# Kernel optimization log

Measured on AMD Instinct MI355X. Metric: run time of the kernel, lower is better.

## Reference

```python
import jax, jax.numpy as jnp
import numpy as np

N, E, D_FEAT, D_HID, N_CLASS, N_LAYER = 100000, 1600000, 128, 128, 40, 2


def _sage_layer(x, x_, src, dst, wl, wr, b, n):
    # mean aggregation of neighbor (src) features into dst nodes
    agg = jax.ops.segment_sum(x[src], dst, num_segments=n)          # [N, d_in]
    cnt = jax.ops.segment_sum(jnp.ones((src.shape[0], 1), x.dtype), dst, num_segments=n)
    agg = agg / jnp.maximum(cnt, 1.0)
    h = agg @ wl + x @ wr + b        # neighbor path + root path
    h_ = x_ @ wr + b                 # twin (detached-root) stream: root weight only
    return jax.nn.relu(h), jax.nn.relu(h_)


def setup_inputs() -> dict:
    key = jax.random.key(0)
    ks = jax.random.split(key, 12)
    s = 1.0 / np.sqrt(D_HID)
    inp = {
        "x": jax.random.normal(ks[0], (N, D_FEAT), jnp.float32),
        "edge_index1": jax.random.randint(ks[1], (2, E), 0, N, jnp.int32),
        "edge_index2": jax.random.randint(ks[2], (2, E), 0, N, jnp.int32),
        "wl1": jax.random.uniform(ks[3], (D_FEAT, D_HID), jnp.float32, -s, s),
        "wr1": jax.random.uniform(ks[4], (D_FEAT, D_HID), jnp.float32, -s, s),
        "b1": jnp.zeros((D_HID,), jnp.float32),
        "wl2": jax.random.uniform(ks[5], (D_HID, D_HID), jnp.float32, -s, s),
        "wr2": jax.random.uniform(ks[6], (D_HID, D_HID), jnp.float32, -s, s),
        "b2": jnp.zeros((D_HID,), jnp.float32),
        "w_out": jax.random.uniform(ks[7], (D_HID * N_LAYER, N_CLASS), jnp.float32, -s, s),
        "b_out": jnp.zeros((N_CLASS,), jnp.float32),
        "batch_size": N,
    }
    return inp


def reference(x, edge_index1, edge_index2, wl1, wr1, b1, wl2, wr2, b2, w_out, b_out, batch_size):
    n = x.shape[0]
    x_ = jax.lax.stop_gradient(x)[:batch_size]   # detached twin stream of root nodes
    # layer 1 (dropout is eval-mode no-op)
    h1, h1_ = _sage_layer(x, x_, edge_index1[0], edge_index1[1], wl1, wr1, b1, n)
    # layer 2
    h2, h2_ = _sage_layer(h1, h1_, edge_index2[0], edge_index2[1], wl2, wr2, b2, n)
    # jumping knowledge: mode 'cat' over per-layer root representations
    h = jnp.concatenate([h1[:batch_size], h2[:batch_size]], axis=-1)
    return h @ w_out + b_out
```

## Files before the change

kernel.cpp:

```cpp
#include <hip/hip_runtime.h>


#define MAXB  512
#define CAP   24
#define CAPS  6144
#define PBLK  384

typedef __attribute__((ext_vector_type(8))) short short8;
typedef __attribute__((ext_vector_type(4))) float floatx4;

__device__ __forceinline__ unsigned short f2b(float f) {
    unsigned u = __float_as_uint(f);
    unsigned r = (u + 0x7fffu + ((u >> 16) & 1u)) >> 16;
    return (unsigned short)r;
}
__device__ __forceinline__ float lo2f(unsigned u) { return __uint_as_float(u << 16); }
__device__ __forceinline__ float hi2f(unsigned u) { return __uint_as_float(u & 0xffff0000u); }
__device__ __forceinline__ unsigned pack2(float a, float b) {
    return (unsigned)f2b(a) | ((unsigned)f2b(b) << 16);
}

__global__ __launch_bounds__(256)
void prep_hist(const float4* __restrict__ x4, uint4* __restrict__ xb4, long n8,
               const float* __restrict__ wl1, const float* __restrict__ wr1,
               const float* __restrict__ wl2, const float* __restrict__ wr2,
               const float* __restrict__ wo,
               unsigned short* __restrict__ wt1, unsigned short* __restrict__ wt2,
               unsigned short* __restrict__ wot,
               const int* __restrict__ dst1, const int* __restrict__ dst2,
               int* __restrict__ hist1, int* __restrict__ hist2, int E, int nb) {
    long i = (long)blockIdx.x * 256 + threadIdx.x;
    if (i < n8) {
        float4 a = x4[i * 2];
        float4 b = x4[i * 2 + 1];
        uint4 o;
        o.x = pack2(a.x, a.y); o.y = pack2(a.z, a.w);
        o.z = pack2(b.x, b.y); o.w = pack2(b.z, b.w);
        xb4[i] = o;
    }
    if (i < 65536) {
        int l = (int)(i >> 15);
        int k5 = (int)(i & 32767);
        int j = k5 & 7, lane = (k5 >> 3) & 63, kb = (k5 >> 9) & 7, c = k5 >> 12;
        int k = kb * 32 + (lane >> 4) * 8 + j;
        int n = c * 16 + (lane & 15);
        const float* Wl = l ? wl2 : wl1;
        const float* Wr = l ? wr2 : wr1;
        float v = (k < 128) ? Wl[k * 128 + n] : Wr[(k - 128) * 128 + n];
        (l ? wt2 : wt1)[k5] = f2b(v);
    } else if (i < 65536 + 12288) {
        int k5 = (int)(i - 65536);
        int j = k5 & 7, lane = (k5 >> 3) & 63, kb = (k5 >> 9) & 7, c = k5 >> 12;
        int k = kb * 32 + (lane >> 4) * 8 + j;
        int col = c * 16 + (lane & 15);
        float v = (col < 40) ? wo[k * 40 + col] : 0.0f;
        wot[k5] = f2b(v);
    }
    __shared__ int h[MAXB];
    if (blockIdx.x < 512) {
        const int layer = blockIdx.x >> 8;
        const int bx    = blockIdx.x & 255;
        const int* dst  = layer ? dst2 : dst1;
        int* hist       = layer ? hist2 : hist1;
        for (int k = threadIdx.x; k < nb; k += 256) h[k] = 0;
        __syncthreads();
        for (int e = bx * 256 + threadIdx.x; e < E; e += 256 * 256)
            atomicAdd(&h[dst[e] >> 8], 1);
        __syncthreads();
        for (int k = threadIdx.x; k < nb; k += 256)
            if (h[k]) atomicAdd(&hist[k], h[k]);
    }
}

__global__ __launch_bounds__(256)
void bucket_scan2(const int* __restrict__ hist1, const int* __restrict__ hist2,
                  int* __restrict__ bptr1, int* __restrict__ bptr2, int nb, int E) {
    __shared__ int pair[256];
    const int* hist = blockIdx.x ? hist2 : hist1;
    int* bptr       = blockIdx.x ? bptr2 : bptr1;
    int t = threadIdx.x;
    int v0 = (2 * t < nb) ? hist[2 * t] : 0;
    int v1 = (2 * t + 1 < nb) ? hist[2 * t + 1] : 0;
    pair[t] = v0 + v1;
    __syncthreads();
    for (int off = 1; off < 256; off <<= 1) {
        int y = (t >= off) ? pair[t - off] : 0;
        __syncthreads();
        pair[t] += y;
        __syncthreads();
    }
    int ebase = pair[t] - (v0 + v1);
    if (2 * t < nb)     bptr[2 * t]     = ebase;
    if (2 * t + 1 < nb) bptr[2 * t + 1] = ebase + v0;
    if (t == 0) bptr[nb] = E;
}

__global__ __launch_bounds__(256)
void partition_edges2(const int* __restrict__ ei1, const int* __restrict__ ei2,
                      const int* __restrict__ bptr1, const int* __restrict__ bptr2,
                      int* __restrict__ gcur1, int* __restrict__ gcur2,
                      int* __restrict__ part1, int* __restrict__ part2,
                      int E, int nb) {
    __shared__ unsigned stage[MAXB][CAP];
    __shared__ int lcnt[MAXB];
    const int* src  = blockIdx.y ? ei2 : ei1;
    const int* dst  = src + E;
    const int* bptr = blockIdx.y ? bptr2 : bptr1;
    int* gcur       = blockIdx.y ? gcur2 : gcur1;
    int* part       = blockIdx.y ? part2 : part1;
    const int t = threadIdx.x;
    for (int i = t; i < nb; i += 256) lcnt[i] = 0;
    __syncthreads();
    const int per = (E + gridDim.x - 1) / gridDim.x;
    const int e0 = blockIdx.x * per;
    const int e1 = min(e0 + per, E);
    for (int e = e0 + t; e < e1; e += 256) {
        int d = dst[e];
        int b = d >> 8;
        unsigned rec = (unsigned)src[e] | ((unsigned)(d & 255) << 17);
        int p = atomicAdd(&lcnt[b], 1);
        if (p < CAP) stage[b][p] = rec;
        else {
            int g = atomicAdd(&gcur[b], 1);
            part[bptr[b] + g] = (int)rec;
        }
    }
    __syncthreads();
    for (int b = t; b < nb; b += 256) {
        int c = lcnt[b]; if (c > CAP) c = CAP;
        if (c > 0) {
            int g = atomicAdd(&gcur[b], c);
            int base = bptr[b] + g;
            for (int i = 0; i < c; ++i) part[base + i] = (int)stage[b][i];
        }
    }
}

__global__ __launch_bounds__(256)
void node_sort2(const int* __restrict__ bptr1, const int* __restrict__ bptr2,
                const int* __restrict__ part1, const int* __restrict__ part2,
                int* __restrict__ col1, int* __restrict__ col2,
                int* __restrict__ row_ptr1, int* __restrict__ row_ptr2,
                int N, int E) {
    __shared__ int recs[CAPS];
    __shared__ int sorted[CAPS];
    __shared__ int hcnt[256];
    __shared__ int hoff[256];
    const int* bptr = blockIdx.y ? bptr2 : bptr1;
    const int* part = blockIdx.y ? part2 : part1;
    int* col        = blockIdx.y ? col2 : col1;
    int* row_ptr    = blockIdx.y ? row_ptr2 : row_ptr1;
    const int b = blockIdx.x, t = threadIdx.x;
    const int beg = bptr[b], end = bptr[b + 1];
    int cnt = end - beg;
    if (cnt > CAPS) cnt = CAPS;

    for (int i = t; i < cnt; i += 256) recs[i] = part[beg + i];
    hcnt[t] = 0;
    __syncthreads();
    for (int i = t; i < cnt; i += 256)
        atomicAdd(&hcnt[((unsigned)recs[i]) >> 17], 1);
    __syncthreads();

    int v = hcnt[t];
    hoff[t] = v;
    __syncthreads();
    for (int off = 1; off < 256; off <<= 1) {
        int y = (t >= off) ? hoff[t - off] : 0;
        __syncthreads();
        hoff[t] += y;
        __syncthreads();
    }
    int myoff = hoff[t] - v;

    int row = b * 256 + t;
    if (row <= N) row_ptr[row] = beg + myoff;
    if (b == gridDim.x - 1 && t == 0) row_ptr[N] = E;
    __syncthreads();
    hoff[t] = myoff;
    hcnt[t] = 0;
    __syncthreads();

    for (int i = t; i < cnt; i += 256) {
        unsigned rec = (unsigned)recs[i];
        int node = rec >> 17;
        int p = hoff[node] + atomicAdd(&hcnt[node], 1);
        sorted[p] = (int)(rec & 0x1FFFF);
    }
    __syncthreads();
    for (int i = t; i < cnt; i += 256) col[beg + i] = sorted[i];
}

__device__ __forceinline__ void gather_node(const uint4* __restrict__ xb,
                                            const int* __restrict__ col,
                                            int beg, int end, int lane,
                                            float acc[8]) {
    int e = beg;
    if (e + 8 <= end) {
        int cidx[8];
#pragma unroll
        for (int q = 0; q < 8; ++q) cidx[q] = col[e + q];
        for (;;) {
            uint4 v[8];
#pragma unroll
            for (int q = 0; q < 8; ++q) v[q] = xb[(size_t)cidx[q] * 16 + lane];
            e += 8;
            const bool more = (e + 8 <= end);
            if (more) {
#pragma unroll
                for (int q = 0; q < 8; ++q) cidx[q] = col[e + q];
            }
#pragma unroll
            for (int q = 0; q < 8; ++q) {
                acc[0] += lo2f(v[q].x); acc[1] += hi2f(v[q].x);
                acc[2] += lo2f(v[q].y); acc[3] += hi2f(v[q].y);
                acc[4] += lo2f(v[q].z); acc[5] += hi2f(v[q].z);
                acc[6] += lo2f(v[q].w); acc[7] += hi2f(v[q].w);
            }
            if (!more) break;
        }
    }
    for (; e + 3 < end; e += 4) {
        uint4 v[4];
#pragma unroll
        for (int q = 0; q < 4; ++q) v[q] = xb[(size_t)col[e + q] * 16 + lane];
#pragma unroll
        for (int q = 0; q < 4; ++q) {
            acc[0] += lo2f(v[q].x); acc[1] += hi2f(v[q].x);
            acc[2] += lo2f(v[q].y); acc[3] += hi2f(v[q].y);
            acc[4] += lo2f(v[q].z); acc[5] += hi2f(v[q].z);
            acc[6] += lo2f(v[q].w); acc[7] += hi2f(v[q].w);
        }
    }
    for (; e < end; ++e) {
        uint4 v0 = xb[(size_t)col[e] * 16 + lane];
        acc[0] += lo2f(v0.x); acc[1] += hi2f(v0.x);
        acc[2] += lo2f(v0.y); acc[3] += hi2f(v0.y);
        acc[4] += lo2f(v0.z); acc[5] += hi2f(v0.z);
        acc[6] += lo2f(v0.w); acc[7] += hi2f(v0.w);
    }
    float inv = 1.0f / fmaxf((float)(end - beg), 1.0f);
#pragma unroll
    for (int j = 0; j < 8; ++j) acc[j] *= inv;
}

#define LDS_SLOT(row, col4) ((row) * 16 + ((col4) ^ ((row) & 7)))

__global__ __launch_bounds__(256)
void fused_layer1(const uint4* __restrict__ xb, const int* __restrict__ row_ptr,
                  const int* __restrict__ col,
                  const unsigned short* __restrict__ Wt,
                  const float* __restrict__ bias,
                  unsigned short* __restrict__ Hb, int N) {
    __shared__ uint4 lds[16 * 16];
    const int t = threadIdx.x;
    {
        const int lrow = t >> 4;
        const int lane = t & 15;
        const int node = blockIdx.x * 16 + lrow;
        float acc[8];
#pragma unroll
        for (int j = 0; j < 8; ++j) acc[j] = 0.0f;
        if (node < N)
            gather_node(xb, col, row_ptr[node], row_ptr[node + 1], lane, acc);
        uint4 o;
        o.x = pack2(acc[0], acc[1]); o.y = pack2(acc[2], acc[3]);
        o.z = pack2(acc[4], acc[5]); o.w = pack2(acc[6], acc[7]);
        lds[LDS_SLOT(lrow, lane)] = o;
    }
    __syncthreads();

    const int wave = t >> 6;
    const int lane = t & 63;
    const int quad = lane >> 4;
    const int l16  = lane & 15;
    const int rowbase = blockIdx.x * 16;

    floatx4 acc2[2] = {(floatx4){0.f,0.f,0.f,0.f}, (floatx4){0.f,0.f,0.f,0.f}};
    int arow = rowbase + l16; if (arow >= N) arow = N - 1;
    const unsigned short* Xs = (const unsigned short*)xb;
    const size_t aoff = (size_t)arow * 128 + quad * 8;

#pragma unroll
    for (int kb = 0; kb < 8; ++kb) {
        short8 a;
        if (kb < 4)
            a = __builtin_bit_cast(short8, lds[LDS_SLOT(l16, quad + (kb & 3) * 4)]);
        else
            a = __builtin_bit_cast(short8, *(const uint4*)(Xs + aoff + (kb & 3) * 32));
#pragma unroll
        for (int cc = 0; cc < 2; ++cc) {
            const int c = wave * 2 + cc;
            short8 b = __builtin_bit_cast(short8,
                *(const uint4*)(Wt + (size_t)(((c * 8 + kb) * 64 + lane) * 8)));
            acc2[cc] = __builtin_amdgcn_mfma_f32_16x16x32_bf16(a, b, acc2[cc], 0, 0, 0);
        }
    }

#pragma unroll
    for (int cc = 0; cc < 2; ++cc) {
        const int c = wave * 2 + cc;
        const float bc = bias[c * 16 + l16];
#pragma unroll
        for (int i = 0; i < 4; ++i) {
            int row = rowbase + quad * 4 + i;
            if (row < N)
                Hb[(size_t)row * 128 + c * 16 + l16] = f2b(fmaxf(acc2[cc][i] + bc, 0.f));
        }
    }
}

__global__ __launch_bounds__(256)
void fused_layer2(const uint4* __restrict__ h1b4, const int* __restrict__ row_ptr,
                  const int* __restrict__ col,
                  const unsigned short* __restrict__ Wt,
                  const float* __restrict__ bias,
                  const unsigned short* __restrict__ Wot,
                  const float* __restrict__ bo,
                  float* __restrict__ out, int N) {
    __shared__ uint4 lds[16 * 16];
    const int t = threadIdx.x;
    {
        const int lrow = t >> 4;
        const int lane = t & 15;
        const int node = blockIdx.x * 16 + lrow;
        float acc[8];
#pragma unroll
        for (int j = 0; j < 8; ++j) acc[j] = 0.0f;
        if (node < N)
            gather_node(h1b4, col, row_ptr[node], row_ptr[node + 1], lane, acc);
        uint4 o;
        o.x = pack2(acc[0], acc[1]); o.y = pack2(acc[2], acc[3]);
        o.z = pack2(acc[4], acc[5]); o.w = pack2(acc[6], acc[7]);
        lds[LDS_SLOT(lrow, lane)] = o;
    }
    __syncthreads();

    const int wave = t >> 6;
    const int lane = t & 63;
    const int quad = lane >> 4;
    const int l16  = lane & 15;
    const int rowbase = blockIdx.x * 16;

    floatx4 acc2[2] = {(floatx4){0.f,0.f,0.f,0.f}, (floatx4){0.f,0.f,0.f,0.f}};
    floatx4 accO    = (floatx4){0.f,0.f,0.f,0.f};
    int arow = rowbase + l16; if (arow >= N) arow = N - 1;
    const unsigned short* H1s = (const unsigned short*)h1b4;
    const size_t aoff = (size_t)arow * 128 + quad * 8;

#pragma unroll
    for (int kb = 0; kb < 8; ++kb) {
        short8 a;
        if (kb < 4)
            a = __builtin_bit_cast(short8, lds[LDS_SLOT(l16, quad + (kb & 3) * 4)]);
        else
            a = __builtin_bit_cast(short8, *(const uint4*)(H1s + aoff + (kb & 3) * 32));
#pragma unroll
        for (int cc = 0; cc < 2; ++cc) {
            const int c = wave * 2 + cc;
            short8 b = __builtin_bit_cast(short8,
                *(const uint4*)(Wt + (size_t)(((c * 8 + kb) * 64 + lane) * 8)));
            acc2[cc] = __builtin_amdgcn_mfma_f32_16x16x32_bf16(a, b, acc2[cc], 0, 0, 0);
        }
        if (kb >= 4 && wave < 3) {
            short8 b = __builtin_bit_cast(short8,
                *(const uint4*)(Wot + (size_t)(((wave * 8 + (kb - 4)) * 64 + lane) * 8)));
            accO = __builtin_amdgcn_mfma_f32_16x16x32_bf16(a, b, accO, 0, 0, 0);
        }
    }

    __syncthreads();
    {
        unsigned short* lds16 = (unsigned short*)lds;
#pragma unroll
        for (int cc = 0; cc < 2; ++cc) {
            const int c = wave * 2 + cc;
            const float bc = bias[c * 16 + l16];
            const int colc = c * 16 + l16;
            const int col4 = colc >> 3;
#pragma unroll
            for (int i = 0; i < 4; ++i) {
                const int lrow = quad * 4 + i;
                lds16[LDS_SLOT(lrow, col4) * 8 + (colc & 7)] =
                    f2b(fmaxf(acc2[cc][i] + bc, 0.f));
            }
        }
    }
    __syncthreads();

    if (wave < 3) {
#pragma unroll
        for (int kh = 0; kh < 4; ++kh) {
            short8 a = __builtin_bit_cast(short8, lds[LDS_SLOT(l16, quad + kh * 4)]);
            short8 b = __builtin_bit_cast(short8,
                *(const uint4*)(Wot + (size_t)(((wave * 8 + 4 + kh) * 64 + lane) * 8)));
            accO = __builtin_amdgcn_mfma_f32_16x16x32_bf16(a, b, accO, 0, 0, 0);
        }
        const int colc = wave * 16 + l16;
        if (colc < 40) {
            const float bco = bo[colc];
#pragma unroll
            for (int i = 0; i < 4; ++i) {
                int row = rowbase + quad * 4 + i;
                if (row < N) out[(size_t)row * 40 + colc] = accO[i] + bco;
            }
        }
    }
}

extern "C" void kernel_launch(void* const* d_in, const int* in_sizes, int n_in,
                              void* d_out, int out_size, void* d_ws, size_t ws_size,
                              hipStream_t stream) {
    const float* x     = (const float*)d_in[0];
    const int*   ei1   = (const int*)d_in[1];
    const int*   ei2   = (const int*)d_in[2];
    const float* wl1   = (const float*)d_in[3];
    const float* wr1   = (const float*)d_in[4];
    const float* b1    = (const float*)d_in[5];
    const float* wl2   = (const float*)d_in[6];
    const float* wr2   = (const float*)d_in[7];
    const float* b2    = (const float*)d_in[8];
    const float* w_out = (const float*)d_in[9];
    const float* b_out = (const float*)d_in[10];

    const int N  = in_sizes[0] / 128;
    const int E  = in_sizes[1] / 2;
    const int nb = (N + 255) >> 8;

    int* hist1    = (int*)d_ws;
    int* gcur1    = hist1 + 512;
    int* hist2    = gcur1 + 512;
    int* gcur2    = hist2 + 512;
    int* bptr1    = gcur2 + 512;
    int* bptr2    = bptr1 + 513;
    int* row_ptr1 = bptr2 + 513;
    int* row_ptr2 = row_ptr1 + (N + 1);
    int* part1    = row_ptr2 + (N + 1);
    int* col1     = part1 + E;
    int* part2    = col1 + E;
    int* col2     = part2 + E;
    size_t int_cnt = (size_t)(2048 + 1026 + 2 * (N + 1)) + (size_t)4 * E;
    int_cnt = (int_cnt + 3) & ~(size_t)3;
    unsigned short* xb   = (unsigned short*)((int*)d_ws + int_cnt);
    unsigned short* h1b  = xb  + (size_t)N * 128;
    unsigned short* wt1  = h1b + (size_t)N * 128;
    unsigned short* wt2  = wt1 + 32768;
    unsigned short* wot  = wt2 + 32768;

    const long n8         = (long)N * 128 / 8;
    const int prep_blocks = (int)((n8 + 255) / 256);
    const int tile_blocks = (N + 15) / 16;

    hipMemsetAsync(hist1, 0, 2048 * sizeof(int), stream);

    prep_hist<<<prep_blocks, 256, 0, stream>>>(
        (const float4*)x, (uint4*)xb, n8, wl1, wr1, wl2, wr2, w_out,
        wt1, wt2, wot, ei1 + E, ei2 + E, hist1, hist2, E, nb);

    bucket_scan2<<<2, 256, 0, stream>>>(hist1, hist2, bptr1, bptr2, nb, E);
    partition_edges2<<<dim3(PBLK, 2), 256, 0, stream>>>(
        ei1, ei2, bptr1, bptr2, gcur1, gcur2, part1, part2, E, nb);
    node_sort2<<<dim3(nb, 2), 256, 0, stream>>>(
        bptr1, bptr2, part1, part2, col1, col2, row_ptr1, row_ptr2, N, E);

    fused_layer1<<<tile_blocks, 256, 0, stream>>>(
        (const uint4*)xb, row_ptr1, col1, wt1, b1, h1b, N);
    fused_layer2<<<tile_blocks, 256, 0, stream>>>(
        (const uint4*)h1b, row_ptr2, col2, wt2, b2, wot, b_out,
        (float*)d_out, N);
}
```

Before: 381.7 us.

## Degree-sort nodes within buckets for balanced tiles and fold bucket scan into prep

Builds a per-bucket permutation of nodes ordered by in-degree so each 16-node tile in the layer kernels processes nodes of similar degree, reducing intra-block load imbalance during neighbor gathering. The separate bucket scan kernel is removed and performed by the last-finishing histogram block using a ticket counter. The partition flush now writes staged records with one wave per bucket in a coalesced way. The permutation makes row writes and root-row loads scattered rather than contiguous per tile.

```diff
diff --git a/kernel.cpp b/kernel.cpp
--- a/kernel.cpp
+++ b/kernel.cpp
@@ -28,7 +28,9 @@
                unsigned short* __restrict__ wt1, unsigned short* __restrict__ wt2,
                unsigned short* __restrict__ wot,
                const int* __restrict__ dst1, const int* __restrict__ dst2,
-               int* __restrict__ hist1, int* __restrict__ hist2, int E, int nb) {
+               int* __restrict__ hist1, int* __restrict__ hist2,
+               int* __restrict__ bptr1, int* __restrict__ bptr2,
+               int* __restrict__ done, int E, int nb) {
     long i = (long)blockIdx.x * 256 + threadIdx.x;
     if (i < n8) {
         float4 a = x4[i * 2];
@@ -57,6 +59,7 @@
         wot[k5] = f2b(v);
     }
     __shared__ int h[MAXB];
+    __shared__ int sticket;
     if (blockIdx.x < 512) {
         const int layer = blockIdx.x >> 8;
         const int bx    = blockIdx.x & 255;
@@ -69,30 +72,33 @@
         __syncthreads();
         for (int k = threadIdx.x; k < nb; k += 256)
             if (h[k]) atomicAdd(&hist[k], h[k]);
-    }
-}
-
-__global__ __launch_bounds__(256)
-void bucket_scan2(const int* __restrict__ hist1, const int* __restrict__ hist2,
-                  int* __restrict__ bptr1, int* __restrict__ bptr2, int nb, int E) {
-    __shared__ int pair[256];
-    const int* hist = blockIdx.x ? hist2 : hist1;
-    int* bptr       = blockIdx.x ? bptr2 : bptr1;
-    int t = threadIdx.x;
-    int v0 = (2 * t < nb) ? hist[2 * t] : 0;
-    int v1 = (2 * t + 1 < nb) ? hist[2 * t + 1] : 0;
-    pair[t] = v0 + v1;
-    __syncthreads();
-    for (int off = 1; off < 256; off <<= 1) {
-        int y = (t >= off) ? pair[t - off] : 0;
-        __syncthreads();
-        pair[t] += y;
-        __syncthreads();
-    }
-    int ebase = pair[t] - (v0 + v1);
-    if (2 * t < nb)     bptr[2 * t]     = ebase;
-    if (2 * t + 1 < nb) bptr[2 * t + 1] = ebase + v0;
-    if (t == 0) bptr[nb] = E;
+        __threadfence();
+        if (threadIdx.x == 0) sticket = atomicAdd(done, 1);
+        __syncthreads();
+        if (sticket == 511) {
+            int* pair = h;
+            const int tt = threadIdx.x;
+            for (int l = 0; l < 2; ++l) {
+                int* hist = l ? hist2 : hist1;
+                int* bptr = l ? bptr2 : bptr1;
+                int v0 = (2 * tt < nb)     ? atomicAdd(&hist[2 * tt], 0)     : 0;
+                int v1 = (2 * tt + 1 < nb) ? atomicAdd(&hist[2 * tt + 1], 0) : 0;
+                pair[tt] = v0 + v1;
+                __syncthreads();
+                for (int off = 1; off < 256; off <<= 1) {
+                    int y = (tt >= off) ? pair[tt - off] : 0;
+                    __syncthreads();
+                    pair[tt] += y;
+                    __syncthreads();
+                }
+                int ebase = pair[tt] - (v0 + v1);
+                if (2 * tt < nb)     bptr[2 * tt]     = ebase;
+                if (2 * tt + 1 < nb) bptr[2 * tt + 1] = ebase + v0;
+                if (tt == 0) bptr[nb] = E;
+                __syncthreads();
+            }
+        }
+    }
 }
 
 __global__ __launch_bounds__(256)
@@ -126,13 +132,15 @@
         }
     }
     __syncthreads();
-    for (int b = t; b < nb; b += 256) {
+    const int wv = t >> 6, ln = t & 63;
+    for (int b = wv; b < nb; b += 4) {
         int c = lcnt[b]; if (c > CAP) c = CAP;
-        if (c > 0) {
-            int g = atomicAdd(&gcur[b], c);
-            int base = bptr[b] + g;
-            for (int i = 0; i < c; ++i) part[base + i] = (int)stage[b][i];
-        }
+        if (c == 0) continue;
+        int g = 0;
+        if (ln == 0) g = atomicAdd(&gcur[b], c);
+        g = __shfl(g, 0, 64);
+        int base = bptr[b] + g;
+        if (ln < c) part[base + ln] = (int)stage[b][ln];
     }
 }
 
@@ -141,15 +149,19 @@
                 const int* __restrict__ part1, const int* __restrict__ part2,
                 int* __restrict__ col1, int* __restrict__ col2,
                 int* __restrict__ row_ptr1, int* __restrict__ row_ptr2,
+                int* __restrict__ nperm1, int* __restrict__ nperm2,
                 int N, int E) {
     __shared__ int recs[CAPS];
     __shared__ int sorted[CAPS];
     __shared__ int hcnt[256];
     __shared__ int hoff[256];
+    __shared__ int dh[64];
+    __shared__ int dcur[64];
     const int* bptr = blockIdx.y ? bptr2 : bptr1;
     const int* part = blockIdx.y ? part2 : part1;
     int* col        = blockIdx.y ? col2 : col1;
     int* row_ptr    = blockIdx.y ? row_ptr2 : row_ptr1;
+    int* nperm      = blockIdx.y ? nperm2 : nperm1;
     const int b = blockIdx.x, t = threadIdx.x;
     const int beg = bptr[b], end = bptr[b + 1];
     int cnt = end - beg;
@@ -189,6 +201,25 @@
     }
     __syncthreads();
     for (int i = t; i < cnt; i += 256) col[beg + i] = sorted[i];
+
+    const int gnode = b * 256 + t;
+    const int bin = (gnode < N) ? min(v, 62) : 63;
+    if (t < 64) dh[t] = 0;
+    __syncthreads();
+    atomicAdd(&dh[bin], 1);
+    __syncthreads();
+    if (t < 64) dcur[t] = dh[t];
+    __syncthreads();
+    for (int off = 1; off < 64; off <<= 1) {
+        int y = (t >= off && t < 64) ? dcur[t - off] : 0;
+        __syncthreads();
+        if (t < 64) dcur[t] += y;
+        __syncthreads();
+    }
+    if (t < 64) dh[t] = dcur[t] - dh[t];
+    __syncthreads();
+    int pos = atomicAdd(&dh[bin], 1);
+    nperm[b * 256 + pos] = gnode;
 }
 
 __device__ __forceinline__ void gather_node(const uint4* __restrict__ xb,
@@ -248,16 +279,19 @@
 
 __global__ __launch_bounds__(256)
 void fused_layer1(const uint4* __restrict__ xb, const int* __restrict__ row_ptr,
-                  const int* __restrict__ col,
+                  const int* __restrict__ col, const int* __restrict__ perm,
                   const unsigned short* __restrict__ Wt,
                   const float* __restrict__ bias,
                   unsigned short* __restrict__ Hb, int N) {
     __shared__ uint4 lds[16 * 16];
+    __shared__ int pnode[16];
     const int t = threadIdx.x;
+    if (t < 16) pnode[t] = perm[blockIdx.x * 16 + t];
+    __syncthreads();
     {
         const int lrow = t >> 4;
         const int lane = t & 15;
-        const int node = blockIdx.x * 16 + lrow;
+        const int node = pnode[lrow];
         float acc[8];
 #pragma unroll
         for (int j = 0; j < 8; ++j) acc[j] = 0.0f;
@@ -274,12 +308,11 @@
     const int lane = t & 63;
     const int quad = lane >> 4;
     const int l16  = lane & 15;
-    const int rowbase = blockIdx.x * 16;
 
     floatx4 acc2[2] = {(floatx4){0.f,0.f,0.f,0.f}, (floatx4){0.f,0.f,0.f,0.f}};
-    int arow = rowbase + l16; if (arow >= N) arow = N - 1;
+    int anode = pnode[l16]; if (anode >= N) anode = 0;
     const unsigned short* Xs = (const unsigned short*)xb;
-    const size_t aoff = (size_t)arow * 128 + quad * 8;
+    const size_t aoff = (size_t)anode * 128 + quad * 8;
 
 #pragma unroll
     for (int kb = 0; kb < 8; ++kb) {
@@ -303,27 +336,30 @@
         const float bc = bias[c * 16 + l16];
 #pragma unroll
         for (int i = 0; i < 4; ++i) {
-            int row = rowbase + quad * 4 + i;
-            if (row < N)
-                Hb[(size_t)row * 128 + c * 16 + l16] = f2b(fmaxf(acc2[cc][i] + bc, 0.f));
+            int rown = pnode[quad * 4 + i];
+            if (rown < N)
+                Hb[(size_t)rown * 128 + c * 16 + l16] = f2b(fmaxf(acc2[cc][i] + bc, 0.f));
         }
     }
 }
 
 __global__ __launch_bounds__(256)
 void fused_layer2(const uint4* __restrict__ h1b4, const int* __restrict__ row_ptr,
-                  const int* __restrict__ col,
+                  const int* __restrict__ col, const int* __restrict__ perm,
                   const unsigned short* __restrict__ Wt,
                   const float* __restrict__ bias,
                   const unsigned short* __restrict__ Wot,
                   const float* __restrict__ bo,
                   float* __restrict__ out, int N) {
     __shared__ uint4 lds[16 * 16];
+    __shared__ int pnode[16];
     const int t = threadIdx.x;
+    if (t < 16) pnode[t] = perm[blockIdx.x * 16 + t];
+    __syncthreads();
     {
         const int lrow = t >> 4;
         const int lane = t & 15;
-        const int node = blockIdx.x * 16 + lrow;
+        const int node = pnode[lrow];
         float acc[8];
 #pragma unroll
         for (int j = 0; j < 8; ++j) acc[j] = 0.0f;
@@ -340,13 +376,12 @@
     const int lane = t & 63;
     const int quad = lane >> 4;
     const int l16  = lane & 15;
-    const int rowbase = blockIdx.x * 16;
 
     floatx4 acc2[2] = {(floatx4){0.f,0.f,0.f,0.f}, (floatx4){0.f,0.f,0.f,0.f}};
     floatx4 accO    = (floatx4){0.f,0.f,0.f,0.f};
-    int arow = rowbase + l16; if (arow >= N) arow = N - 1;
+    int anode = pnode[l16]; if (anode >= N) anode = 0;
     const unsigned short* H1s = (const unsigned short*)h1b4;
-    const size_t aoff = (size_t)arow * 128 + quad * 8;
+    const size_t aoff = (size_t)anode * 128 + quad * 8;
 
 #pragma unroll
     for (int kb = 0; kb < 8; ++kb) {
@@ -401,8 +436,8 @@
             const float bco = bo[colc];
 #pragma unroll
             for (int i = 0; i < 4; ++i) {
-                int row = rowbase + quad * 4 + i;
-                if (row < N) out[(size_t)row * 40 + colc] = accO[i] + bco;
+                int rown = pnode[quad * 4 + i];
+                if (rown < N) out[(size_t)rown * 40 + colc] = accO[i] + bco;
             }
         }
     }
@@ -439,7 +474,11 @@
     int* col1     = part1 + E;
     int* part2    = col1 + E;
     int* col2     = part2 + E;
-    size_t int_cnt = (size_t)(2048 + 1026 + 2 * (N + 1)) + (size_t)4 * E;
+    int* nperm1   = col2 + E;
+    int* nperm2   = nperm1 + (size_t)nb * 256;
+    int* done     = gcur2 + 511;
+    size_t int_cnt = (size_t)(2048 + 1026 + 2 * (N + 1)) + (size_t)4 * E
+                   + (size_t)2 * nb * 256;
     int_cnt = (int_cnt + 3) & ~(size_t)3;
     unsigned short* xb   = (unsigned short*)((int*)d_ws + int_cnt);
     unsigned short* h1b  = xb  + (size_t)N * 128;
@@ -455,17 +494,18 @@
 
     prep_hist<<<prep_blocks, 256, 0, stream>>>(
         (const float4*)x, (uint4*)xb, n8, wl1, wr1, wl2, wr2, w_out,
-        wt1, wt2, wot, ei1 + E, ei2 + E, hist1, hist2, E, nb);
-
-    bucket_scan2<<<2, 256, 0, stream>>>(hist1, hist2, bptr1, bptr2, nb, E);
+        wt1, wt2, wot, ei1 + E, ei2 + E, hist1, hist2, bptr1, bptr2,
+        done, E, nb);
+
     partition_edges2<<<dim3(PBLK, 2), 256, 0, stream>>>(
         ei1, ei2, bptr1, bptr2, gcur1, gcur2, part1, part2, E, nb);
     node_sort2<<<dim3(nb, 2), 256, 0, stream>>>(
-        bptr1, bptr2, part1, part2, col1, col2, row_ptr1, row_ptr2, N, E);
+        bptr1, bptr2, part1, part2, col1, col2, row_ptr1, row_ptr2,
+        nperm1, nperm2, N, E);
 
     fused_layer1<<<tile_blocks, 256, 0, stream>>>(
-        (const uint4*)xb, row_ptr1, col1, wt1, b1, h1b, N);
+        (const uint4*)xb, row_ptr1, col1, nperm1, wt1, b1, h1b, N);
     fused_layer2<<<tile_blocks, 256, 0, stream>>>(
-        (const uint4*)h1b, row_ptr2, col2, wt2, b2, wot, b_out,
+        (const uint4*)h1b, row_ptr2, col2, nperm2, wt2, b2, wot, b_out,
         (float*)d_out, N);
 }
```

New measurement: 965.4 us. +152.9%, slower.

## Fold bucket scan into histogram kernel; sort CSR columns by source within rows

Applied to the files above, without the earlier changes.

Removes the separate bucket_scan2 launch by having the last-finishing histogram block, chosen through an atomic ticket counter, compute the bucket prefix sums. The flush in partition_edges is rewritten so each wavefront writes a bucket's staged records in parallel instead of one thread looping over them. node_sort now uses a 16384-bin histogram keyed by destination node plus the high source bits, so edges within each row are roughly ordered by source index for better gather locality in the fused layers. This adds a larger shared-memory footprint and a serial 64-bin scan per thread, and it relies on the 'done' counter being zeroed by the existing memset.

```diff
diff --git a/kernel.cpp b/kernel.cpp
--- a/kernel.cpp
+++ b/kernel.cpp
@@ -5,6 +5,7 @@
 #define CAP   24
 #define CAPS  6144
 #define PBLK  384
+#define NBINS 16384
 
 typedef __attribute__((ext_vector_type(8))) short short8;
 typedef __attribute__((ext_vector_type(4))) float floatx4;
@@ -28,7 +29,9 @@
                unsigned short* __restrict__ wt1, unsigned short* __restrict__ wt2,
                unsigned short* __restrict__ wot,
                const int* __restrict__ dst1, const int* __restrict__ dst2,
-               int* __restrict__ hist1, int* __restrict__ hist2, int E, int nb) {
+               int* __restrict__ hist1, int* __restrict__ hist2,
+               int* __restrict__ bptr1, int* __restrict__ bptr2,
+               int* __restrict__ done, int E, int nb) {
     long i = (long)blockIdx.x * 256 + threadIdx.x;
     if (i < n8) {
         float4 a = x4[i * 2];
@@ -57,6 +60,7 @@
         wot[k5] = f2b(v);
     }
     __shared__ int h[MAXB];
+    __shared__ int sticket;
     if (blockIdx.x < 512) {
         const int layer = blockIdx.x >> 8;
         const int bx    = blockIdx.x & 255;
@@ -69,30 +73,33 @@
         __syncthreads();
         for (int k = threadIdx.x; k < nb; k += 256)
             if (h[k]) atomicAdd(&hist[k], h[k]);
-    }
-}
-
-__global__ __launch_bounds__(256)
-void bucket_scan2(const int* __restrict__ hist1, const int* __restrict__ hist2,
-                  int* __restrict__ bptr1, int* __restrict__ bptr2, int nb, int E) {
-    __shared__ int pair[256];
-    const int* hist = blockIdx.x ? hist2 : hist1;
-    int* bptr       = blockIdx.x ? bptr2 : bptr1;
-    int t = threadIdx.x;
-    int v0 = (2 * t < nb) ? hist[2 * t] : 0;
-    int v1 = (2 * t + 1 < nb) ? hist[2 * t + 1] : 0;
-    pair[t] = v0 + v1;
-    __syncthreads();
-    for (int off = 1; off < 256; off <<= 1) {
-        int y = (t >= off) ? pair[t - off] : 0;
+        __threadfence();
+        if (threadIdx.x == 0) sticket = atomicAdd(done, 1);
         __syncthreads();
-        pair[t] += y;
-        __syncthreads();
-    }
-    int ebase = pair[t] - (v0 + v1);
-    if (2 * t < nb)     bptr[2 * t]     = ebase;
-    if (2 * t + 1 < nb) bptr[2 * t + 1] = ebase + v0;
-    if (t == 0) bptr[nb] = E;
+        if (sticket == 511) {
+            int* pair = h;
+            const int tt = threadIdx.x;
+            for (int l = 0; l < 2; ++l) {
+                int* hist = l ? hist2 : hist1;
+                int* bptr = l ? bptr2 : bptr1;
+                int v0 = (2 * tt < nb)     ? atomicAdd(&hist[2 * tt], 0)     : 0;
+                int v1 = (2 * tt + 1 < nb) ? atomicAdd(&hist[2 * tt + 1], 0) : 0;
+                pair[tt] = v0 + v1;
+                __syncthreads();
+                for (int off = 1; off < 256; off <<= 1) {
+                    int y = (tt >= off) ? pair[tt - off] : 0;
+                    __syncthreads();
+                    pair[tt] += y;
+                    __syncthreads();
+                }
+                int ebase = pair[tt] - (v0 + v1);
+                if (2 * tt < nb)     bptr[2 * tt]     = ebase;
+                if (2 * tt + 1 < nb) bptr[2 * tt + 1] = ebase + v0;
+                if (tt == 0) bptr[nb] = E;
+                __syncthreads();
+            }
+        }
+    }
 }
 
 __global__ __launch_bounds__(256)
@@ -103,6 +110,7 @@
                       int E, int nb) {
     __shared__ unsigned stage[MAXB][CAP];
     __shared__ int lcnt[MAXB];
+    __shared__ int sbase[MAXB];
     const int* src  = blockIdx.y ? ei2 : ei1;
     const int* dst  = src + E;
     const int* bptr = blockIdx.y ? bptr2 : bptr1;
@@ -128,11 +136,13 @@
     __syncthreads();
     for (int b = t; b < nb; b += 256) {
         int c = lcnt[b]; if (c > CAP) c = CAP;
-        if (c > 0) {
-            int g = atomicAdd(&gcur[b], c);
-            int base = bptr[b] + g;
-            for (int i = 0; i < c; ++i) part[base + i] = (int)stage[b][i];
-        }
+        if (c > 0) sbase[b] = bptr[b] + atomicAdd(&gcur[b], c);
+    }
+    __syncthreads();
+    const int wv = t >> 6, ln = t & 63;
+    for (int b = wv; b < nb; b += 4) {
+        int c = lcnt[b]; if (c > CAP) c = CAP;
+        if (ln < c) part[sbase[b] + ln] = (int)stage[b][ln];
     }
 }
 
@@ -144,8 +154,8 @@
                 int N, int E) {
     __shared__ int recs[CAPS];
     __shared__ int sorted[CAPS];
-    __shared__ int hcnt[256];
-    __shared__ int hoff[256];
+    __shared__ int hist[NBINS];
+    __shared__ int wpart[256];
     const int* bptr = blockIdx.y ? bptr2 : bptr1;
     const int* part = blockIdx.y ? part2 : part1;
     int* col        = blockIdx.y ? col2 : col1;
@@ -156,36 +166,42 @@
     if (cnt > CAPS) cnt = CAPS;
 
     for (int i = t; i < cnt; i += 256) recs[i] = part[beg + i];
-    hcnt[t] = 0;
-    __syncthreads();
-    for (int i = t; i < cnt; i += 256)
-        atomicAdd(&hcnt[((unsigned)recs[i]) >> 17], 1);
-    __syncthreads();
-
-    int v = hcnt[t];
-    hoff[t] = v;
-    __syncthreads();
-    for (int off = 1; off < 256; off <<= 1) {
-        int y = (t >= off) ? hoff[t - off] : 0;
-        __syncthreads();
-        hoff[t] += y;
-        __syncthreads();
-    }
-    int myoff = hoff[t] - v;
-
-    int row = b * 256 + t;
-    if (row <= N) row_ptr[row] = beg + myoff;
-    if (b == gridDim.x - 1 && t == 0) row_ptr[N] = E;
-    __syncthreads();
-    hoff[t] = myoff;
-    hcnt[t] = 0;
-    __syncthreads();
-
+    for (int i = t; i < NBINS; i += 256) hist[i] = 0;
+    __syncthreads();
     for (int i = t; i < cnt; i += 256) {
         unsigned rec = (unsigned)recs[i];
-        int node = rec >> 17;
-        int p = hoff[node] + atomicAdd(&hcnt[node], 1);
-        sorted[p] = (int)(rec & 0x1FFFF);
+        int key = (int)((rec >> 17) << 6) | (int)((rec & 0x1FFFFu) >> 11);
+        atomicAdd(&hist[key], 1);
+    }
+    __syncthreads();
+
+    const int base = t * 64;
+    int s = 0;
+#pragma unroll 8
+    for (int j = 0; j < 64; ++j) { int v = hist[base + j]; hist[base + j] = s; s += v; }
+    wpart[t] = s;
+    __syncthreads();
+    for (int off = 1; off < 256; off <<= 1) {
+        int y = (t >= off) ? wpart[t - off] : 0;
+        __syncthreads();
+        wpart[t] += y;
+        __syncthreads();
+    }
+    const int excl = wpart[t] - s;
+#pragma unroll 8
+    for (int j = 0; j < 64; ++j) hist[base + j] += excl;
+    __syncthreads();
+
+    int row = b * 256 + t;
+    if (row <= N) row_ptr[row] = beg + hist[t * 64];
+    if (b == gridDim.x - 1 && t == 0) row_ptr[N] = E;
+    __syncthreads();
+
+    for (int i = t; i < cnt; i += 256) {
+        unsigned rec = (unsigned)recs[i];
+        int key = (int)((rec >> 17) << 6) | (int)((rec & 0x1FFFFu) >> 11);
+        int p = atomicAdd(&hist[key], 1);
+        sorted[p] = (int)(rec & 0x1FFFFu);
     }
     __syncthreads();
     for (int i = t; i < cnt; i += 256) col[beg + i] = sorted[i];
@@ -439,6 +455,7 @@
     int* col1     = part1 + E;
     int* part2    = col1 + E;
     int* col2     = part2 + E;
+    int* done     = gcur2 + 511;
     size_t int_cnt = (size_t)(2048 + 1026 + 2 * (N + 1)) + (size_t)4 * E;
     int_cnt = (int_cnt + 3) & ~(size_t)3;
     unsigned short* xb   = (unsigned short*)((int*)d_ws + int_cnt);
@@ -455,9 +472,9 @@
 
     prep_hist<<<prep_blocks, 256, 0, stream>>>(
         (const float4*)x, (uint4*)xb, n8, wl1, wr1, wl2, wr2, w_out,
-        wt1, wt2, wot, ei1 + E, ei2 + E, hist1, hist2, E, nb);
-
-    bucket_scan2<<<2, 256, 0, stream>>>(hist1, hist2, bptr1, bptr2, nb, E);
+        wt1, wt2, wot, ei1 + E, ei2 + E, hist1, hist2, bptr1, bptr2,
+        done, E, nb);
+
     partition_edges2<<<dim3(PBLK, 2), 256, 0, stream>>>(
         ei1, ei2, bptr1, bptr2, gcur1, gcur2, part1, part2, E, nb);
     node_sort2<<<dim3(nb, 2), 256, 0, stream>>>(
```

Result: slower. 457.6 us (+19.9%).
